# Kernel optimization log

Measured on AMD Instinct MI355X. Metric: run time of the kernel, lower is better.

The kernel has to match this reference:

```python
import jax, jax.numpy as jnp
import numpy as np

B, LQ, LK, H = 8, 2048, 2048, 1024


def setup_inputs() -> dict:
    key = jax.random.key(0)
    kq, kk, kv, km, kw = jax.random.split(key, 5)
    input_Q = jax.random.normal(kq, (B, LQ, H), dtype=jnp.float32)
    input_K = jax.random.normal(kk, (B, LK, H), dtype=jnp.float32)
    input_V = jax.random.normal(kv, (B, LK, H), dtype=jnp.float32)
    mask = jax.random.randint(km, (B, LK), 0, 2, dtype=jnp.int32)
    # learned parameter w_omega [H, H]; scaled init so scores are O(1)-ish
    w_omega = jax.random.normal(kw, (H, H), dtype=jnp.float32) * (H ** -0.5)
    return {"input_Q": input_Q, "input_K": input_K, "input_V": input_V,
            "w_omega": w_omega, "mask": mask}


def reference(input_Q, input_K, input_V, w_omega, mask):
    # att_input = Q @ W : [B, Lq, H]
    att_input = jnp.einsum('bqh,hd->bqd', input_Q, w_omega)
    # scores = att_input @ K^T : [B, Lq, Lk]
    att_scores = jnp.einsum('bqd,bkd->bqk', att_input, input_K)
    # masked fill with -inf where mask == 0 (mask broadcast over query dim)
    neg_inf = jnp.asarray(-jnp.inf, dtype=att_scores.dtype)
    scores = jnp.where(mask[:, None, :] == 0, neg_inf, att_scores)
    probs_softmax = jax.nn.softmax(scores, axis=-1)          # [B, Lq, Lk]
    probs_sigmoid = jax.nn.sigmoid(scores)                   # sigmoid(-inf)=0
    probs_sigmoid_hat = (probs_sigmoid > 0.5).astype(probs_softmax.dtype)
    att_output_softmax = jnp.einsum('bqk,bkh->bqh', probs_softmax, input_V)
    att_output_sigmoid = jnp.einsum('bqk,bkh->bqh', probs_sigmoid_hat, input_V)
    # torch .squeeze(1) is a no-op here since Lq > 1
    return (att_output_softmax, att_output_sigmoid, probs_softmax, probs_sigmoid)
```

## Files before the change

kernel.cpp:

```cpp
#include <hip/hip_runtime.h>
#include <math.h>

#define B_  8
#define LQ_ 2048
#define LK_ 2048
#define H_  1024

#define TAU      4e-3f
#define FIX_CAP  32768
#define FIX_E    8
#define SCL      256.0f
#define SCLQ     16.0f
#define INV_SS   (1.0f / 1048576.0f)

#define KBLK 512

typedef unsigned short ushort_t;
typedef __attribute__((ext_vector_type(8))) _Float16 v8h;
typedef __attribute__((ext_vector_type(8))) short  v8s;
typedef __attribute__((ext_vector_type(4))) float  v4f;
typedef __attribute__((ext_vector_type(4))) float  f4;
typedef __attribute__((ext_vector_type(4))) int    i4;
typedef __attribute__((ext_vector_type(4))) short  s4;

#if defined(__has_builtin)
#if __has_builtin(__builtin_amdgcn_global_load_lds)
#define HAS_GLDS 1
#endif
#endif

__device__ __forceinline__ ushort_t f2bf(float x) {
  unsigned u = __float_as_uint(x);
  u = (u + 0x7FFFu + ((u >> 16) & 1u)) >> 16;
  return (ushort_t)u;
}
__device__ __forceinline__ void split2h(float x, ushort_t& h, ushort_t& l) {
  union { _Float16 f; ushort_t u; } a, b;
  a.f = (_Float16)x;
  b.f = (_Float16)(x - (float)a.f);
  h = a.u; l = b.u;
}

__device__ __forceinline__ void gld_lds16(void* lds_dst, const void* g_src) {
#ifdef HAS_GLDS
  __builtin_amdgcn_global_load_lds((const __attribute__((address_space(1))) void*)g_src,
                                   (__attribute__((address_space(3))) void*)lds_dst,
                                   16, 0, 0);
#else
  *(i4*)lds_dst = *(const i4*)g_src;
#endif
}

__device__ __forceinline__ void xcd_remap(int& bx, int& by, int& bz) {
  const int nx = gridDim.x, ny = gridDim.y;
  const int nwg = nx * ny * gridDim.z;
  const int hwid = bx + nx * (by + ny * bz);
  const int work = (hwid & 7) * (nwg >> 3) + (hwid >> 3);
  bx = work % nx;
  const int t = work / nx;
  by = t % ny;
  bz = t / ny;
}

__global__ void k_zero(int* p) { *p = 0; }

__global__ void k_split(const float* __restrict__ x, ushort_t* __restrict__ hi,
                        ushort_t* __restrict__ lo, int n4, float scale) {
  int stride = gridDim.x * blockDim.x;
  for (int i = blockIdx.x * blockDim.x + threadIdx.x; i < n4; i += stride) {
    f4 v = ((const f4*)x)[i];
    s4 h, l;
#pragma unroll
    for (int j = 0; j < 4; j++) {
      ushort_t hb, lb; split2h(v[j] * scale, hb, lb);
      h[j] = (short)hb; l[j] = (short)lb;
    }
    ((s4*)hi)[i] = h;
    ((s4*)lo)[i] = l;
  }
}

template <int SPLIT>
__global__ void k_transpose(const float* __restrict__ X, ushort_t* __restrict__ Yhi,
                            ushort_t* __restrict__ Ylo, int R, int C, float scale) {
  __shared__ float t[32][33];
  const int b = blockIdx.z;
  const float* Xb = X + (size_t)b * R * C;
  ushort_t* Yh = Yhi + (size_t)b * R * C;
  const int c0 = blockIdx.x * 32, r0 = blockIdx.y * 32;
  const int tx = threadIdx.x, ty = threadIdx.y;
#pragma unroll
  for (int i = 0; i < 4; i++)
    t[ty + 8 * i][tx] = Xb[(size_t)(r0 + ty + 8 * i) * C + c0 + tx];
  __syncthreads();
#pragma unroll
  for (int i = 0; i < 4; i++) {
    float v = t[tx][ty + 8 * i] * scale;
    size_t o = (size_t)(c0 + ty + 8 * i) * R + r0 + tx;
    if (SPLIT) {
      ushort_t h, l; split2h(v, h, l);
      Yh[o] = h;
      (Ylo + (size_t)b * R * C)[o] = l;
    } else {
      Yh[o] = f2bf(v);
    }
  }
}


template <int EPI>
__global__ __launch_bounds__(256, 2)
void gemm_hx2(const ushort_t* __restrict__ Ahi, const ushort_t* __restrict__ Alo,
              const ushort_t* __restrict__ Bhi, const ushort_t* __restrict__ Blo,
              int KD, long strideAB, long strideBB, int N,
              ushort_t* __restrict__ OutHi, ushort_t* __restrict__ OutLo, long strideOB,
              float* __restrict__ S, float* __restrict__ G, ushort_t* __restrict__ Hatb,
              const int* __restrict__ mask, int* __restrict__ cnt, int* __restrict__ flist) {
  int bx = blockIdx.x, by = blockIdx.y, bz = blockIdx.z;
  xcd_remap(bx, by, bz);
  const int b  = bz;
  const int m0 = by * 128;
  const int n0 = bx * 128;
  const ushort_t* Ah = Ahi + (size_t)b * strideAB + (size_t)m0 * KD;
  const ushort_t* Al = Alo + (size_t)b * strideAB + (size_t)m0 * KD;
  const ushort_t* Bh = Bhi + (size_t)b * strideBB + (size_t)n0 * KD;
  const ushort_t* Bl = Blo + (size_t)b * strideBB + (size_t)n0 * KD;

  __shared__ ushort_t sAh[128 * 32], sAl[128 * 32], sBh[128 * 32], sBl[128 * 32];

  const int tid  = threadIdx.x;
  const int lane = tid & 63;
  const int wid  = tid >> 6;
  const int wm   = (wid >> 1) * 64;
  const int wn   = (wid & 1) * 64;

  v4f acc[4][4] = {};

  const int r1 = tid >> 2;
  const int c1 = (tid & 3) ^ ((tid >> 3) & 3);
  const size_t go1 = (size_t)r1 * KD + (size_t)(c1 * 8);
  const size_t go2 = (size_t)(r1 + 64) * KD + (size_t)(c1 * 8);
  const int ldst1 = tid * 16;
  const int ldst2 = 4096 + tid * 16;

  const int fr = lane & 15;
  const int cq = lane >> 4;

  for (int k0 = 0; k0 < KD; k0 += 32) {
    __syncthreads();
    gld_lds16((char*)sAh + ldst1, Ah + go1 + k0);
    gld_lds16((char*)sAh + ldst2, Ah + go2 + k0);
    gld_lds16((char*)sAl + ldst1, Al + go1 + k0);
    gld_lds16((char*)sAl + ldst2, Al + go2 + k0);
    gld_lds16((char*)sBh + ldst1, Bh + go1 + k0);
    gld_lds16((char*)sBh + ldst2, Bh + go2 + k0);
    gld_lds16((char*)sBl + ldst1, Bl + go1 + k0);
    gld_lds16((char*)sBl + ldst2, Bl + go2 + k0);
    __syncthreads();

    v8h a_h[4], a_l[4], b_h[4], b_l[4];
#pragma unroll
    for (int i = 0; i < 4; i++) {
      const int Ra = wm + i * 16 + fr;
      const int ca = Ra * 32 + (((cq ^ ((Ra >> 1) & 3))) << 3);
      a_h[i] = *(const v8h*)&sAh[ca];
      a_l[i] = *(const v8h*)&sAl[ca];
      const int Rb = wn + i * 16 + fr;
      const int cb = Rb * 32 + (((cq ^ ((Rb >> 1) & 3))) << 3);
      b_h[i] = *(const v8h*)&sBh[cb];
      b_l[i] = *(const v8h*)&sBl[cb];
    }
#pragma unroll
    for (int i = 0; i < 4; i++)
#pragma unroll
      for (int j = 0; j < 4; j++) {
        acc[i][j] = __builtin_amdgcn_mfma_f32_16x16x32_f16(a_h[i], b_h[j], acc[i][j], 0, 0, 0);
        acc[i][j] = __builtin_amdgcn_mfma_f32_16x16x32_f16(a_h[i], b_l[j], acc[i][j], 0, 0, 0);
        acc[i][j] = __builtin_amdgcn_mfma_f32_16x16x32_f16(a_l[i], b_h[j], acc[i][j], 0, 0, 0);
      }
  }

  const int rg = (lane >> 4) * 4;
#pragma unroll
  for (int i = 0; i < 4; i++)
#pragma unroll
    for (int j = 0; j < 4; j++)
#pragma unroll
      for (int r = 0; r < 4; r++) {
        const int grow = m0 + wm + i * 16 + rg + r;
        const int gcol = n0 + wn + j * 16 + fr;
        const float v = acc[i][j][r];
        if (EPI == 0) {
          size_t o = (size_t)b * strideOB + (size_t)grow * N + gcol;
          ushort_t h, l; split2h(v, h, l);
          OutHi[o] = h; OutLo[o] = l;
        } else {
          size_t o = ((size_t)b * LQ_ + grow) * N + gcol;
          const float sv = v * INV_SS;
          S[o] = sv;
          int mk = mask[b * N + gcol];
          const float g = mk ? 1.0f / (1.0f + expf(-sv)) : 0.0f;
          G[o] = g;
          Hatb[o] = (g > 0.5f) ? (ushort_t)0x3F80 : (ushort_t)0;
          if (mk && fabsf(sv) < TAU) {
            int idx = atomicAdd(cnt, 1);
            if (idx < FIX_CAP) flist[idx] = (b << 22) | (grow << 11) | gcol;
          }
        }
      }
}

__global__ __launch_bounds__(256)
void k_fix_blas(const int* __restrict__ cnt, const int* __restrict__ flist,
                const float* __restrict__ Q, const float* __restrict__ Kx,
                const float* __restrict__ W, float* __restrict__ S,
                float* __restrict__ G, ushort_t* __restrict__ Hatb) {
  const int n = min(*cnt, FIX_CAP);
  const int base = blockIdx.x * FIX_E;
  if (base >= n) return;
  const int ne = min(FIX_E, n - base);
  const int tid = threadIdx.x;

  __shared__ float qs[FIX_E][H_];
  __shared__ float aA[FIX_E][H_];
  __shared__ int   ent[FIX_E];

  if (tid < FIX_E) ent[tid] = flist[base + ((tid < ne) ? tid : 0)];
  __syncthreads();

  for (int e = 0; e < FIX_E; e++) {
    const int en = ent[e];
    const int b = en >> 22, q = (en >> 11) & 2047;
    const float* Qr = Q + ((size_t)b * LQ_ + q) * H_;
    for (int i = tid; i < H_; i += 256) qs[e][i] = Qr[i];
  }
  __syncthreads();

  float atot[FIX_E][4];
  float acc[FIX_E][4];
  const float* Wp = W + tid * 4;
#pragma unroll
  for (int blk = 0; blk < 2; blk++) {
    const int h0 = blk * KBLK;
    const int h1 = h0 + KBLK;
#pragma unroll
    for (int e = 0; e < FIX_E; e++)
#pragma unroll
      for (int j = 0; j < 4; j++) acc[e][j] = 0.f;
    for (int h = h0; h < h1; h++) {
      f4 w = *(const f4*)(Wp + (size_t)h * H_);
#pragma unroll
      for (int e = 0; e < FIX_E; e++) {
        const float qv = qs[e][h];
        acc[e][0] = fmaf(qv, w[0], acc[e][0]);
        acc[e][1] = fmaf(qv, w[1], acc[e][1]);
        acc[e][2] = fmaf(qv, w[2], acc[e][2]);
        acc[e][3] = fmaf(qv, w[3], acc[e][3]);
      }
    }
#pragma unroll
    for (int e = 0; e < FIX_E; e++)
#pragma unroll
      for (int j = 0; j < 4; j++)
        atot[e][j] = (blk == 0) ? acc[e][j] : __fadd_rn(atot[e][j], acc[e][j]);
  }
#pragma unroll
  for (int e = 0; e < FIX_E; e++) {
    aA[e][tid * 4 + 0] = atot[e][0];
    aA[e][tid * 4 + 1] = atot[e][1];
    aA[e][tid * 4 + 2] = atot[e][2];
    aA[e][tid * 4 + 3] = atot[e][3];
  }
  __syncthreads();

  if (tid < ne) {
    const int e = tid;
    const int en = ent[e];
    const int b = en >> 22, q = (en >> 11) & 2047, k = en & 2047;
    const float* Kr = Kx + ((size_t)b * LK_ + k) * H_;
    const float* Ar = aA[e];
    float stot = 0.f;
#pragma unroll
    for (int blk = 0; blk < 2; blk++) {
      const int d0 = blk * KBLK;
      const int d1 = d0 + KBLK;
      float a = 0.f;
#pragma unroll 16
      for (int d = d0; d < d1; d++) a = fmaf(Ar[d], Kr[d], a);
      stot = (blk == 0) ? a : __fadd_rn(stot, a);
    }
    size_t o = ((size_t)b * LQ_ + q) * LK_ + k;
    S[o] = stot;
    const float g = 1.0f / (1.0f + expf(-stot));
    G[o] = g;
    Hatb[o] = (g > 0.5f) ? (ushort_t)0x3F80 : (ushort_t)0;
  }
}

__global__ void k_softmax(float* __restrict__ S, const int* __restrict__ mask,
                          ushort_t* __restrict__ Pb) {
  const int row = blockIdx.x;
  const int b   = row >> 11;
  float* Sr = S + (size_t)row * LK_;
  const int* mr = mask + b * LK_;
  const int tid = threadIdx.x;
  const int c0 = tid * 8;

  float v[8]; int mk[8];
  f4 v0 = *(const f4*)&Sr[c0];
  f4 v1 = *(const f4*)&Sr[c0 + 4];
  i4 m0 = *(const i4*)&mr[c0];
  i4 m1 = *(const i4*)&mr[c0 + 4];
#pragma unroll
  for (int j = 0; j < 4; j++) { v[j] = v0[j]; v[4 + j] = v1[j]; mk[j] = m0[j]; mk[4 + j] = m1[j]; }

  float mx = -INFINITY;
#pragma unroll
  for (int j = 0; j < 8; j++) if (mk[j]) mx = fmaxf(mx, v[j]);
#pragma unroll
  for (int off = 32; off; off >>= 1) mx = fmaxf(mx, __shfl_xor(mx, off));
  __shared__ float redm[4], reds[4];
  const int lane = tid & 63, wid = tid >> 6;
  if (lane == 0) redm[wid] = mx;
  __syncthreads();
  mx = fmaxf(fmaxf(redm[0], redm[1]), fmaxf(redm[2], redm[3]));

  float e[8], sum = 0.f;
#pragma unroll
  for (int j = 0; j < 8; j++) { e[j] = mk[j] ? expf(v[j] - mx) : 0.f; sum += e[j]; }
#pragma unroll
  for (int off = 32; off; off >>= 1) sum += __shfl_xor(sum, off);
  if (lane == 0) reds[wid] = sum;
  __syncthreads();
  sum = reds[0] + reds[1] + reds[2] + reds[3];
  const float inv = 1.0f / sum;

  f4 o0, o1;
  v8s pb;
#pragma unroll
  for (int j = 0; j < 4; j++) {
    o0[j] = e[j] * inv; o1[j] = e[4 + j] * inv;
    pb[j] = (short)f2bf(o0[j]); pb[4 + j] = (short)f2bf(o1[j]);
  }
  *(f4*)&Sr[c0] = o0;
  *(f4*)&Sr[c0 + 4] = o1;
  *(v8s*)&Pb[(size_t)row * LK_ + c0] = pb;
}

__global__ __launch_bounds__(256, 2)
void gemm_pv2(const ushort_t* __restrict__ P, const ushort_t* __restrict__ Hb,
              const ushort_t* __restrict__ Bt,
              float* __restrict__ O0, float* __restrict__ O1) {
  int bx = blockIdx.x, by = blockIdx.y, bz = blockIdx.z;
  xcd_remap(bx, by, bz);
  const int b  = bz;
  const int m0 = by * 128;
  const int n0 = bx * 128;
  const ushort_t* Pa = P  + ((size_t)b * LQ_ + m0) * (size_t)LK_;
  const ushort_t* Ha = Hb + ((size_t)b * LQ_ + m0) * (size_t)LK_;
  const ushort_t* Bb = Bt + ((size_t)b * H_  + n0) * (size_t)LK_;

  __shared__ ushort_t sP[128 * 32], sH[128 * 32], sB[128 * 32];

  const int tid  = threadIdx.x;
  const int lane = tid & 63;
  const int wid  = tid >> 6;
  const int wm   = (wid >> 1) * 64;
  const int wn   = (wid & 1) * 64;

  v4f acc0[4][4] = {}, acc1[4][4] = {};

  const int r1 = tid >> 2;
  const int c1 = (tid & 3) ^ ((tid >> 3) & 3);
  const size_t go1 = (size_t)r1 * LK_ + (size_t)(c1 * 8);
  const size_t go2 = (size_t)(r1 + 64) * LK_ + (size_t)(c1 * 8);
  const int ldst1 = tid * 16;
  const int ldst2 = 4096 + tid * 16;

  const int fr = lane & 15;
  const int cq = lane >> 4;

  for (int k0 = 0; k0 < LK_; k0 += 32) {
    __syncthreads();
    gld_lds16((char*)sP + ldst1, Pa + go1 + k0);
    gld_lds16((char*)sP + ldst2, Pa + go2 + k0);
    gld_lds16((char*)sH + ldst1, Ha + go1 + k0);
    gld_lds16((char*)sH + ldst2, Ha + go2 + k0);
    gld_lds16((char*)sB + ldst1, Bb + go1 + k0);
    gld_lds16((char*)sB + ldst2, Bb + go2 + k0);
    __syncthreads();

    v8s pf[4], hf[4], bf[4];
#pragma unroll
    for (int i = 0; i < 4; i++) {
      const int Ra = wm + i * 16 + fr;
      const int ca = Ra * 32 + ((cq ^ ((Ra >> 1) & 3)) << 3);
      pf[i] = *(const v8s*)&sP[ca];
      hf[i] = *(const v8s*)&sH[ca];
      const int Rb = wn + i * 16 + fr;
      bf[i] = *(const v8s*)&sB[Rb * 32 + ((cq ^ ((Rb >> 1) & 3)) << 3)];
    }
#pragma unroll
    for (int i = 0; i < 4; i++)
#pragma unroll
      for (int j = 0; j < 4; j++) {
        acc0[i][j] = __builtin_amdgcn_mfma_f32_16x16x32_bf16(pf[i], bf[j], acc0[i][j], 0, 0, 0);
        acc1[i][j] = __builtin_amdgcn_mfma_f32_16x16x32_bf16(hf[i], bf[j], acc1[i][j], 0, 0, 0);
      }
  }

  const int rg = (lane >> 4) * 4;
#pragma unroll
  for (int i = 0; i < 4; i++)
#pragma unroll
    for (int j = 0; j < 4; j++)
#pragma unroll
      for (int r = 0; r < 4; r++) {
        const int grow = m0 + wm + i * 16 + rg + r;
        const int gcol = n0 + wn + j * 16 + fr;
        const size_t o = ((size_t)b * LQ_ + grow) * H_ + gcol;
        O0[o] = acc0[i][j][r];
        O1[o] = acc1[i][j][r];
      }
}

extern "C" void kernel_launch(void* const* d_in, const int* in_sizes, int n_in,
                              void* d_out, int out_size, void* d_ws, size_t ws_size,
                              hipStream_t stream) {
  const float* Q = (const float*)d_in[0];
  const float* K = (const float*)d_in[1];
  const float* V = (const float*)d_in[2];
  const float* W = (const float*)d_in[3];
  const int* mask = (const int*)d_in[4];

  float* out0 = (float*)d_out;
  float* out1 = out0 + (size_t)B_ * LQ_ * H_;
  float* out2 = out1 + (size_t)B_ * LQ_ * H_;
  float* out3 = out2 + (size_t)B_ * LQ_ * LK_;

  const size_t NQ = (size_t)B_ * LQ_ * H_;
  char* ws = (char*)d_ws;
  int* cnt   = (int*)ws;                    ws += 256;
  int* flist = (int*)ws;                    ws += FIX_CAP * 4;
  ushort_t* Qhi = (ushort_t*)ws;            ws += NQ * 2;
  ushort_t* Qlo = (ushort_t*)ws;            ws += NQ * 2;
  ushort_t* Khi = (ushort_t*)ws;            ws += NQ * 2;
  ushort_t* Klo = (ushort_t*)ws;            ws += NQ * 2;
  ushort_t* Ahi = (ushort_t*)ws;            ws += NQ * 2;
  ushort_t* Alo = (ushort_t*)ws;            ws += NQ * 2;
  ushort_t* Vt  = (ushort_t*)ws;            ws += NQ * 2;
  ushort_t* Wthi = (ushort_t*)ws;           ws += (size_t)H_ * H_ * 2;
  ushort_t* Wtlo = (ushort_t*)ws;

  ushort_t* hatb = Qhi;
  ushort_t* Pb   = Ahi;

  k_zero<<<1, 1, 0, stream>>>(cnt);

  k_split<<<2048, 256, 0, stream>>>(Q, Qhi, Qlo, (int)(NQ / 4), SCLQ);
  k_split<<<2048, 256, 0, stream>>>(K, Khi, Klo, (int)(NQ / 4), SCL);
  dim3 tb(32, 8);
  k_transpose<1><<<dim3(32, 32, 1), tb, 0, stream>>>(W, Wthi, Wtlo, H_, H_, SCL);
  k_transpose<0><<<dim3(32, 64, B_), tb, 0, stream>>>(V, Vt, nullptr, LK_, H_, 1.0f);

  gemm_hx2<0><<<dim3(H_ / 128, LQ_ / 128, B_), 256, 0, stream>>>(
      Qhi, Qlo, Wthi, Wtlo, H_, (long)LQ_ * H_, 0L, H_,
      Ahi, Alo, (long)LQ_ * H_, nullptr, nullptr, nullptr, nullptr, nullptr, nullptr);

  gemm_hx2<1><<<dim3(LK_ / 128, LQ_ / 128, B_), 256, 0, stream>>>(
      Ahi, Alo, Khi, Klo, H_, (long)LQ_ * H_, (long)LK_ * H_, LK_,
      nullptr, nullptr, 0L, out2, out3, hatb, mask, cnt, flist);

  k_fix_blas<<<FIX_CAP / FIX_E, 256, 0, stream>>>(cnt, flist, Q, K, W, out2, out3, hatb);

  k_softmax<<<B_ * LQ_, 256, 0, stream>>>(out2, mask, Pb);

  gemm_pv2<<<dim3(H_ / 128, LQ_ / 128, B_), 256, 0, stream>>>(Pb, hatb, Vt, out0, out1);
}
```

Before: 927.5 us.

## Double-buffer LDS tiles in hx2 and PV GEMM kernels to overlap loads

Both MFMA GEMM kernels now use two LDS buffers. The next K-slice is prefetched with direct global-to-LDS loads while the current slice is read and multiplied, and one of the two barriers per iteration is removed. The goal is to hide global-load latency behind MFMA work. In exchange, LDS use per block doubles (64 KB for hx2), which could limit occupancy at two blocks per CU.

```diff
diff --git a/kernel.cpp b/kernel.cpp
--- a/kernel.cpp
+++ b/kernel.cpp
@@ -126,7 +126,7 @@
   const ushort_t* Bh = Bhi + (size_t)b * strideBB + (size_t)n0 * KD;
   const ushort_t* Bl = Blo + (size_t)b * strideBB + (size_t)n0 * KD;
 
-  __shared__ ushort_t sAh[128 * 32], sAl[128 * 32], sBh[128 * 32], sBl[128 * 32];
+  __shared__ ushort_t sAh[2 * 4096], sAl[2 * 4096], sBh[2 * 4096], sBl[2 * 4096];
 
   const int tid  = threadIdx.x;
   const int lane = tid & 63;
@@ -146,27 +146,35 @@
   const int fr = lane & 15;
   const int cq = lane >> 4;
 
+#define STAGE_HX2(buf, kk)                                              \
+  do {                                                                  \
+    const int bo = (buf) * 8192;                                        \
+    gld_lds16((char*)sAh + bo + ldst1, Ah + go1 + (kk));                \
+    gld_lds16((char*)sAh + bo + ldst2, Ah + go2 + (kk));                \
+    gld_lds16((char*)sAl + bo + ldst1, Al + go1 + (kk));                \
+    gld_lds16((char*)sAl + bo + ldst2, Al + go2 + (kk));                \
+    gld_lds16((char*)sBh + bo + ldst1, Bh + go1 + (kk));                \
+    gld_lds16((char*)sBh + bo + ldst2, Bh + go2 + (kk));                \
+    gld_lds16((char*)sBl + bo + ldst1, Bl + go1 + (kk));                \
+    gld_lds16((char*)sBl + bo + ldst2, Bl + go2 + (kk));                \
+  } while (0)
+
+  STAGE_HX2(0, 0);
+  int cur = 0;
   for (int k0 = 0; k0 < KD; k0 += 32) {
     __syncthreads();
-    gld_lds16((char*)sAh + ldst1, Ah + go1 + k0);
-    gld_lds16((char*)sAh + ldst2, Ah + go2 + k0);
-    gld_lds16((char*)sAl + ldst1, Al + go1 + k0);
-    gld_lds16((char*)sAl + ldst2, Al + go2 + k0);
-    gld_lds16((char*)sBh + ldst1, Bh + go1 + k0);
-    gld_lds16((char*)sBh + ldst2, Bh + go2 + k0);
-    gld_lds16((char*)sBl + ldst1, Bl + go1 + k0);
-    gld_lds16((char*)sBl + ldst2, Bl + go2 + k0);
-    __syncthreads();
-
+    if (k0 + 32 < KD) STAGE_HX2(cur ^ 1, k0 + 32);
+
+    const int off = cur * 4096;
     v8h a_h[4], a_l[4], b_h[4], b_l[4];
 #pragma unroll
     for (int i = 0; i < 4; i++) {
       const int Ra = wm + i * 16 + fr;
-      const int ca = Ra * 32 + (((cq ^ ((Ra >> 1) & 3))) << 3);
+      const int ca = off + Ra * 32 + (((cq ^ ((Ra >> 1) & 3))) << 3);
       a_h[i] = *(const v8h*)&sAh[ca];
       a_l[i] = *(const v8h*)&sAl[ca];
       const int Rb = wn + i * 16 + fr;
-      const int cb = Rb * 32 + (((cq ^ ((Rb >> 1) & 3))) << 3);
+      const int cb = off + Rb * 32 + (((cq ^ ((Rb >> 1) & 3))) << 3);
       b_h[i] = *(const v8h*)&sBh[cb];
       b_l[i] = *(const v8h*)&sBl[cb];
     }
@@ -178,7 +186,9 @@
         acc[i][j] = __builtin_amdgcn_mfma_f32_16x16x32_f16(a_h[i], b_l[j], acc[i][j], 0, 0, 0);
         acc[i][j] = __builtin_amdgcn_mfma_f32_16x16x32_f16(a_l[i], b_h[j], acc[i][j], 0, 0, 0);
       }
-  }
+    cur ^= 1;
+  }
+#undef STAGE_HX2
 
   const int rg = (lane >> 4) * 4;
 #pragma unroll
@@ -360,7 +370,7 @@
   const ushort_t* Ha = Hb + ((size_t)b * LQ_ + m0) * (size_t)LK_;
   const ushort_t* Bb = Bt + ((size_t)b * H_  + n0) * (size_t)LK_;
 
-  __shared__ ushort_t sP[128 * 32], sH[128 * 32], sB[128 * 32];
+  __shared__ ushort_t sP[2 * 4096], sH[2 * 4096], sB[2 * 4096];
 
   const int tid  = threadIdx.x;
   const int lane = tid & 63;
@@ -380,25 +390,33 @@
   const int fr = lane & 15;
   const int cq = lane >> 4;
 
+#define STAGE_PV(buf, kk)                                        \
+  do {                                                           \
+    const int bo = (buf) * 8192;                                 \
+    gld_lds16((char*)sP + bo + ldst1, Pa + go1 + (kk));          \
+    gld_lds16((char*)sP + bo + ldst2, Pa + go2 + (kk));          \
+    gld_lds16((char*)sH + bo + ldst1, Ha + go1 + (kk));          \
+    gld_lds16((char*)sH + bo + ldst2, Ha + go2 + (kk));          \
+    gld_lds16((char*)sB + bo + ldst1, Bb + go1 + (kk));          \
+    gld_lds16((char*)sB + bo + ldst2, Bb + go2 + (kk));          \
+  } while (0)
+
+  STAGE_PV(0, 0);
+  int cur = 0;
   for (int k0 = 0; k0 < LK_; k0 += 32) {
     __syncthreads();
-    gld_lds16((char*)sP + ldst1, Pa + go1 + k0);
-    gld_lds16((char*)sP + ldst2, Pa + go2 + k0);
-    gld_lds16((char*)sH + ldst1, Ha + go1 + k0);
-    gld_lds16((char*)sH + ldst2, Ha + go2 + k0);
-    gld_lds16((char*)sB + ldst1, Bb + go1 + k0);
-    gld_lds16((char*)sB + ldst2, Bb + go2 + k0);
-    __syncthreads();
-
+    if (k0 + 32 < LK_) STAGE_PV(cur ^ 1, k0 + 32);
+
+    const int off = cur * 4096;
     v8s pf[4], hf[4], bf[4];
 #pragma unroll
     for (int i = 0; i < 4; i++) {
       const int Ra = wm + i * 16 + fr;
-      const int ca = Ra * 32 + ((cq ^ ((Ra >> 1) & 3)) << 3);
+      const int ca = off + Ra * 32 + ((cq ^ ((Ra >> 1) & 3)) << 3);
       pf[i] = *(const v8s*)&sP[ca];
       hf[i] = *(const v8s*)&sH[ca];
       const int Rb = wn + i * 16 + fr;
-      bf[i] = *(const v8s*)&sB[Rb * 32 + ((cq ^ ((Rb >> 1) & 3)) << 3)];
+      bf[i] = *(const v8s*)&sB[off + Rb * 32 + ((cq ^ ((Rb >> 1) & 3)) << 3)];
     }
 #pragma unroll
     for (int i = 0; i < 4; i++)
@@ -407,7 +425,9 @@
         acc0[i][j] = __builtin_amdgcn_mfma_f32_16x16x32_bf16(pf[i], bf[j], acc0[i][j], 0, 0, 0);
         acc1[i][j] = __builtin_amdgcn_mfma_f32_16x16x32_bf16(hf[i], bf[j], acc1[i][j], 0, 0, 0);
       }
-  }
+    cur ^= 1;
+  }
+#undef STAGE_PV
 
   const int rg = (lane >> 4) * 4;
 #pragma unroll
```

Measured after the change: 910.1 us. Within noise of the previous version (-1.9%).

## Pipeline GEMMs with triple-buffered async LDS loads and wider 128x256 tiles

Applied to the files above, without the earlier changes.

Rewrites the split-fp16 score GEMMs and the PV GEMM to use 512-thread blocks computing 128x256 tiles, staged through a three-deep LDS ring. Global-to-LDS loads for tile t+2 are issued while tile t is computed, and the old double __syncthreads is replaced by vmcnt waits and a single barrier. MFMA sections run at raised wave priority. This is meant to hide global-load latency and cut barrier stalls, at the cost of large LDS use (144KB and 96KB per block), which limits occupancy to one block per CU.

```diff
diff --git a/kernel.cpp b/kernel.cpp
--- a/kernel.cpp
+++ b/kernel.cpp
@@ -61,6 +61,10 @@
   by = t % ny;
   bz = t / ny;
 }
+
+#define WAIT_VM(n) asm volatile("s_waitcnt vmcnt(" #n ")" ::: "memory")
+#define WAIT_LGKM0() do { asm volatile("s_waitcnt lgkmcnt(0)" ::: "memory"); \
+                          __builtin_amdgcn_sched_barrier(0); } while (0)
 
 __global__ void k_zero(int* p) { *p = 0; }
 
@@ -109,67 +113,77 @@
 
 
 template <int EPI>
-__global__ __launch_bounds__(256, 2)
-void gemm_hx2(const ushort_t* __restrict__ Ahi, const ushort_t* __restrict__ Alo,
-              const ushort_t* __restrict__ Bhi, const ushort_t* __restrict__ Blo,
-              int KD, long strideAB, long strideBB, int N,
-              ushort_t* __restrict__ OutHi, ushort_t* __restrict__ OutLo, long strideOB,
-              float* __restrict__ S, float* __restrict__ G, ushort_t* __restrict__ Hatb,
-              const int* __restrict__ mask, int* __restrict__ cnt, int* __restrict__ flist) {
+__global__ __launch_bounds__(512, 1)
+void gemm_hx2p(const ushort_t* __restrict__ Ahi, const ushort_t* __restrict__ Alo,
+               const ushort_t* __restrict__ Bhi, const ushort_t* __restrict__ Blo,
+               int KD, long strideAB, long strideBB, int N,
+               ushort_t* __restrict__ OutHi, ushort_t* __restrict__ OutLo, long strideOB,
+               float* __restrict__ S, float* __restrict__ G, ushort_t* __restrict__ Hatb,
+               const int* __restrict__ mask, int* __restrict__ cnt, int* __restrict__ flist) {
   int bx = blockIdx.x, by = blockIdx.y, bz = blockIdx.z;
   xcd_remap(bx, by, bz);
   const int b  = bz;
   const int m0 = by * 128;
-  const int n0 = bx * 128;
+  const int n0 = bx * 256;
   const ushort_t* Ah = Ahi + (size_t)b * strideAB + (size_t)m0 * KD;
   const ushort_t* Al = Alo + (size_t)b * strideAB + (size_t)m0 * KD;
   const ushort_t* Bh = Bhi + (size_t)b * strideBB + (size_t)n0 * KD;
   const ushort_t* Bl = Blo + (size_t)b * strideBB + (size_t)n0 * KD;
 
-  __shared__ ushort_t sAh[128 * 32], sAl[128 * 32], sBh[128 * 32], sBl[128 * 32];
+  __shared__ __attribute__((aligned(16))) char lds[3 * 49152];
 
   const int tid  = threadIdx.x;
   const int lane = tid & 63;
-  const int wid  = tid >> 6;
-  const int wm   = (wid >> 1) * 64;
-  const int wn   = (wid & 1) * 64;
+  const int w    = tid >> 6;
+  const int wm   = (w >> 2) * 64;
+  const int wn   = (w & 3) * 64;
+  const int fr   = lane & 15;
+  const int cq   = lane >> 4;
 
   v4f acc[4][4] = {};
 
-  const int r1 = tid >> 2;
-  const int c1 = (tid & 3) ^ ((tid >> 3) & 3);
-  const size_t go1 = (size_t)r1 * KD + (size_t)(c1 * 8);
-  const size_t go2 = (size_t)(r1 + 64) * KD + (size_t)(c1 * 8);
-  const int ldst1 = tid * 16;
-  const int ldst2 = 4096 + tid * 16;
-
-  const int fr = lane & 15;
-  const int cq = lane >> 4;
-
-  for (int k0 = 0; k0 < KD; k0 += 32) {
-    __syncthreads();
-    gld_lds16((char*)sAh + ldst1, Ah + go1 + k0);
-    gld_lds16((char*)sAh + ldst2, Ah + go2 + k0);
-    gld_lds16((char*)sAl + ldst1, Al + go1 + k0);
-    gld_lds16((char*)sAl + ldst2, Al + go2 + k0);
-    gld_lds16((char*)sBh + ldst1, Bh + go1 + k0);
-    gld_lds16((char*)sBh + ldst2, Bh + go2 + k0);
-    gld_lds16((char*)sBl + ldst1, Bl + go1 + k0);
-    gld_lds16((char*)sBl + ldst2, Bl + go2 + k0);
-    __syncthreads();
-
+  const int r4 = tid >> 2;
+  const int gc = (tid & 3) ^ ((r4 >> 1) & 3);
+  const size_t goA  = (size_t)r4 * KD + gc * 8;
+  const size_t goB1 = (size_t)(r4 + 128) * KD + gc * 8;
+  const int lo16 = tid * 16;
+
+#define STG_HX(t_) do {                                                  \
+    char* sb = lds + ((t_) % 3) * 49152;                                 \
+    const int kk = (t_) * 32;                                            \
+    gld_lds16(sb + lo16,                 Ah + goA  + kk);                \
+    gld_lds16(sb + 8192 + lo16,          Al + goA  + kk);                \
+    gld_lds16(sb + 16384 + lo16,         Bh + goA  + kk);                \
+    gld_lds16(sb + 24576 + lo16,         Bh + goB1 + kk);                \
+    gld_lds16(sb + 32768 + lo16,         Bl + goA  + kk);                \
+    gld_lds16(sb + 40960 + lo16,         Bl + goB1 + kk);                \
+  } while (0)
+
+  const int nT = KD / 32;
+  STG_HX(0);
+  STG_HX(1);
+  for (int t = 0; t < nT; ++t) {
+    if (t + 1 < nT) WAIT_VM(6);
+    else            WAIT_VM(0);
+    __builtin_amdgcn_s_barrier();
+
+    const char* sb = lds + (t % 3) * 49152;
     v8h a_h[4], a_l[4], b_h[4], b_l[4];
 #pragma unroll
     for (int i = 0; i < 4; i++) {
       const int Ra = wm + i * 16 + fr;
-      const int ca = Ra * 32 + (((cq ^ ((Ra >> 1) & 3))) << 3);
-      a_h[i] = *(const v8h*)&sAh[ca];
-      a_l[i] = *(const v8h*)&sAl[ca];
+      const int oa = Ra * 64 + ((cq ^ ((Ra >> 1) & 3)) << 4);
+      a_h[i] = *(const v8h*)(sb + oa);
+      a_l[i] = *(const v8h*)(sb + 8192 + oa);
       const int Rb = wn + i * 16 + fr;
-      const int cb = Rb * 32 + (((cq ^ ((Rb >> 1) & 3))) << 3);
-      b_h[i] = *(const v8h*)&sBh[cb];
-      b_l[i] = *(const v8h*)&sBl[cb];
+      const int ob = Rb * 64 + ((cq ^ ((Rb >> 1) & 3)) << 4);
+      b_h[i] = *(const v8h*)(sb + 16384 + ob);
+      b_l[i] = *(const v8h*)(sb + 32768 + ob);
     }
+    if (t + 2 < nT) STG_HX(t + 2);
+
+    WAIT_LGKM0();
+    __builtin_amdgcn_s_setprio(1);
 #pragma unroll
     for (int i = 0; i < 4; i++)
 #pragma unroll
@@ -178,7 +192,9 @@
         acc[i][j] = __builtin_amdgcn_mfma_f32_16x16x32_f16(a_h[i], b_l[j], acc[i][j], 0, 0, 0);
         acc[i][j] = __builtin_amdgcn_mfma_f32_16x16x32_f16(a_l[i], b_h[j], acc[i][j], 0, 0, 0);
       }
-  }
+    __builtin_amdgcn_s_setprio(0);
+  }
+#undef STG_HX
 
   const int rg = (lane >> 4) * 4;
 #pragma unroll
@@ -347,59 +363,69 @@
   *(v8s*)&Pb[(size_t)row * LK_ + c0] = pb;
 }
 
-__global__ __launch_bounds__(256, 2)
-void gemm_pv2(const ushort_t* __restrict__ P, const ushort_t* __restrict__ Hb,
-              const ushort_t* __restrict__ Bt,
-              float* __restrict__ O0, float* __restrict__ O1) {
+__global__ __launch_bounds__(512, 1)
+void gemm_pv2p(const ushort_t* __restrict__ P, const ushort_t* __restrict__ Hb,
+               const ushort_t* __restrict__ Bt,
+               float* __restrict__ O0, float* __restrict__ O1) {
   int bx = blockIdx.x, by = blockIdx.y, bz = blockIdx.z;
   xcd_remap(bx, by, bz);
   const int b  = bz;
   const int m0 = by * 128;
-  const int n0 = bx * 128;
+  const int n0 = bx * 256;
   const ushort_t* Pa = P  + ((size_t)b * LQ_ + m0) * (size_t)LK_;
   const ushort_t* Ha = Hb + ((size_t)b * LQ_ + m0) * (size_t)LK_;
   const ushort_t* Bb = Bt + ((size_t)b * H_  + n0) * (size_t)LK_;
 
-  __shared__ ushort_t sP[128 * 32], sH[128 * 32], sB[128 * 32];
+  __shared__ __attribute__((aligned(16))) char lds[3 * 32768];
 
   const int tid  = threadIdx.x;
   const int lane = tid & 63;
-  const int wid  = tid >> 6;
-  const int wm   = (wid >> 1) * 64;
-  const int wn   = (wid & 1) * 64;
+  const int w    = tid >> 6;
+  const int wm   = (w >> 2) * 64;
+  const int wn   = (w & 3) * 64;
+  const int fr   = lane & 15;
+  const int cq   = lane >> 4;
 
   v4f acc0[4][4] = {}, acc1[4][4] = {};
 
-  const int r1 = tid >> 2;
-  const int c1 = (tid & 3) ^ ((tid >> 3) & 3);
-  const size_t go1 = (size_t)r1 * LK_ + (size_t)(c1 * 8);
-  const size_t go2 = (size_t)(r1 + 64) * LK_ + (size_t)(c1 * 8);
-  const int ldst1 = tid * 16;
-  const int ldst2 = 4096 + tid * 16;
-
-  const int fr = lane & 15;
-  const int cq = lane >> 4;
-
-  for (int k0 = 0; k0 < LK_; k0 += 32) {
-    __syncthreads();
-    gld_lds16((char*)sP + ldst1, Pa + go1 + k0);
-    gld_lds16((char*)sP + ldst2, Pa + go2 + k0);
-    gld_lds16((char*)sH + ldst1, Ha + go1 + k0);
-    gld_lds16((char*)sH + ldst2, Ha + go2 + k0);
-    gld_lds16((char*)sB + ldst1, Bb + go1 + k0);
-    gld_lds16((char*)sB + ldst2, Bb + go2 + k0);
-    __syncthreads();
-
+  const int r4 = tid >> 2;
+  const int gc = (tid & 3) ^ ((r4 >> 1) & 3);
+  const size_t goA  = (size_t)r4 * LK_ + gc * 8;
+  const size_t goB1 = (size_t)(r4 + 128) * LK_ + gc * 8;
+  const int lo16 = tid * 16;
+
+#define STG_PV(t_) do {                                                  \
+    char* sb = lds + ((t_) % 3) * 32768;                                 \
+    const int kk = (t_) * 32;                                            \
+    gld_lds16(sb + lo16,          Pa + goA  + kk);                       \
+    gld_lds16(sb + 8192 + lo16,   Ha + goA  + kk);                       \
+    gld_lds16(sb + 16384 + lo16,  Bb + goA  + kk);                       \
+    gld_lds16(sb + 24576 + lo16,  Bb + goB1 + kk);                       \
+  } while (0)
+
+  const int nT = LK_ / 32;
+  STG_PV(0);
+  STG_PV(1);
+  for (int t = 0; t < nT; ++t) {
+    if (t + 1 < nT) WAIT_VM(4);
+    else            WAIT_VM(0);
+    __builtin_amdgcn_s_barrier();
+
+    const char* sb = lds + (t % 3) * 32768;
     v8s pf[4], hf[4], bf[4];
 #pragma unroll
     for (int i = 0; i < 4; i++) {
       const int Ra = wm + i * 16 + fr;
-      const int ca = Ra * 32 + ((cq ^ ((Ra >> 1) & 3)) << 3);
-      pf[i] = *(const v8s*)&sP[ca];
-      hf[i] = *(const v8s*)&sH[ca];
+      const int oa = Ra * 64 + ((cq ^ ((Ra >> 1) & 3)) << 4);
+      pf[i] = *(const v8s*)(sb + oa);
+      hf[i] = *(const v8s*)(sb + 8192 + oa);
       const int Rb = wn + i * 16 + fr;
-      bf[i] = *(const v8s*)&sB[Rb * 32 + ((cq ^ ((Rb >> 1) & 3)) << 3)];
+      bf[i] = *(const v8s*)(sb + 16384 + Rb * 64 + ((cq ^ ((Rb >> 1) & 3)) << 4));
     }
+    if (t + 2 < nT) STG_PV(t + 2);
+
+    WAIT_LGKM0();
+    __builtin_amdgcn_s_setprio(1);
 #pragma unroll
     for (int i = 0; i < 4; i++)
 #pragma unroll
@@ -407,7 +433,9 @@
         acc0[i][j] = __builtin_amdgcn_mfma_f32_16x16x32_bf16(pf[i], bf[j], acc0[i][j], 0, 0, 0);
         acc1[i][j] = __builtin_amdgcn_mfma_f32_16x16x32_bf16(hf[i], bf[j], acc1[i][j], 0, 0, 0);
       }
-  }
+    __builtin_amdgcn_s_setprio(0);
+  }
+#undef STG_PV
 
   const int rg = (lane >> 4) * 4;
 #pragma unroll
@@ -463,11 +491,11 @@
   k_transpose<1><<<dim3(32, 32, 1), tb, 0, stream>>>(W, Wthi, Wtlo, H_, H_, SCL);
   k_transpose<0><<<dim3(32, 64, B_), tb, 0, stream>>>(V, Vt, nullptr, LK_, H_, 1.0f);
 
-  gemm_hx2<0><<<dim3(H_ / 128, LQ_ / 128, B_), 256, 0, stream>>>(
+  gemm_hx2p<0><<<dim3(H_ / 256, LQ_ / 128, B_), 512, 0, stream>>>(
       Qhi, Qlo, Wthi, Wtlo, H_, (long)LQ_ * H_, 0L, H_,
       Ahi, Alo, (long)LQ_ * H_, nullptr, nullptr, nullptr, nullptr, nullptr, nullptr);
 
-  gemm_hx2<1><<<dim3(LK_ / 128, LQ_ / 128, B_), 256, 0, stream>>>(
+  gemm_hx2p<1><<<dim3(LK_ / 256, LQ_ / 128, B_), 512, 0, stream>>>(
       Ahi, Alo, Khi, Klo, H_, (long)LQ_ * H_, (long)LK_ * H_, LK_,
       nullptr, nullptr, 0L, out2, out3, hatb, mask, cnt, flist);
 
@@ -475,5 +503,5 @@
 
   k_softmax<<<B_ * LQ_, 256, 0, stream>>>(out2, mask, Pb);
 
-  gemm_pv2<<<dim3(H_ / 128, LQ_ / 128, B_), 256, 0, stream>>>(Pb, hatb, Vt, out0, out1);
-}
+  gemm_pv2p<<<dim3(H_ / 256, LQ_ / 128, B_), 512, 0, stream>>>(Pb, hatb, Vt, out0, out1);
+}
```

Result: faster. 850.7 us (-8.3%).
